# Performance work log

Hardware: AMD Instinct MI355X
Metric: run time of the kernel (lower is better)

The kernel has to match this reference:

```python
import jax, jax.numpy as jnp
import numpy as np

N = 50000
E = 800000
EPS = 1e-16
NEG_SLOPE = 0.2

def setup_inputs() -> dict:
    key = jax.random.key(0)
    ks = jax.random.split(key, 10)
    s = lambda fan: 1.0 / np.sqrt(fan)
    return {
        "x": jax.random.normal(ks[0], (N, 128), dtype=jnp.float32),
        "edge_index": jax.random.randint(ks[1], (2, E), 0, N, dtype=jnp.int64),
        "W1": jax.random.normal(ks[2], (128, 4 * 32), dtype=jnp.float32) * s(128),
        "att_src1": jax.random.normal(ks[3], (4, 32), dtype=jnp.float32) * s(32),
        "att_dst1": jax.random.normal(ks[4], (4, 32), dtype=jnp.float32) * s(32),
        "b1": jnp.zeros((128,), dtype=jnp.float32),
        "W2": jax.random.normal(ks[5], (128, 2), dtype=jnp.float32) * s(128),
        "att_src2": jax.random.normal(ks[6], (1, 2), dtype=jnp.float32) * s(2),
        "att_dst2": jax.random.normal(ks[7], (1, 2), dtype=jnp.float32) * s(2),
        "b2": jnp.zeros((2,), dtype=jnp.float32),
    }

def _gat_conv(x, src, dst, W, att_src, att_dst, bias, heads, out_ch, concat):
    n = x.shape[0]
    h = (x @ W).reshape(n, heads, out_ch)                      # [N,H,C]
    a_src = jnp.sum(h * att_src[None], axis=-1)                # [N,H]
    a_dst = jnp.sum(h * att_dst[None], axis=-1)                # [N,H]
    e = jax.nn.leaky_relu(a_src[src] + a_dst[dst], NEG_SLOPE)  # [Etot,H]
    # segment softmax over incoming edges per destination node
    m = jax.ops.segment_max(e, dst, num_segments=n)            # [N,H]
    m = jnp.where(jnp.isfinite(m), m, 0.0)
    ex = jnp.exp(e - m[dst])
    denom = jax.ops.segment_sum(ex, dst, num_segments=n)       # [N,H]
    alpha = ex / (denom[dst] + EPS)                            # [Etot,H]
    out = jax.ops.segment_sum(alpha[:, :, None] * h[src], dst, num_segments=n)  # [N,H,C]
    if concat:
        out = out.reshape(n, heads * out_ch)
    else:
        out = out.mean(axis=1)
    return out + bias

def reference(x, edge_index, W1, att_src1, att_dst1, b1, W2, att_src2, att_dst2, b2):
    n = x.shape[0]
    # PyG GATConv adds self-loops by default
    loops = jnp.arange(n, dtype=edge_index.dtype)
    src = jnp.concatenate([edge_index[0], loops])
    dst = jnp.concatenate([edge_index[1], loops])
    # dropout is identity at inference
    h = jax.nn.elu(_gat_conv(x, src, dst, W1, att_src1, att_dst1, b1, 4, 32, True))
    h = _gat_conv(h, src, dst, W2, att_src2, att_dst2, b2, 1, 2, False)
    return jax.nn.log_softmax(h, axis=1)
```

## Files before the change

kernel.cpp:

```cpp
#include <hip/hip_runtime.h>
#include <hip/hip_bf16.h>

#define NN 50000
#define EE 800000
#define CAP 64
#define NEG_SLOPE 0.2f
#define EPSF 1e-16f
#define BUILD_BLOCKS 1024
#define GEMM_BLOCKS ((NN + 63) / 64)
#define NPAIRS (EE / 2)
#define WROW 136

typedef unsigned int uint32;
typedef __attribute__((ext_vector_type(8))) short short8;
typedef __attribute__((ext_vector_type(4))) float floatx4;

__device__ __forceinline__ unsigned short f2bf(float f) {
  unsigned int u = __float_as_uint(f);
  unsigned int r = (u + 0x7fffu + ((u >> 16) & 1u)) >> 16;
  return (unsigned short)r;
}
__device__ __forceinline__ float bf_lo(uint32 v) { return __uint_as_float(v << 16); }
__device__ __forceinline__ float bf_hi(uint32 v) { return __uint_as_float(v & 0xffff0000u); }
__device__ __forceinline__ float lrelu(float e) { return fmaxf(e, NEG_SLOPE * e); }

__device__ __forceinline__ void do_build(int b, const int* __restrict__ ei,
                                         int* __restrict__ counts,
                                         int* __restrict__ csr) {
  const int range = b & 7;
  const int lo = range * (NN / 8);
  const int hi = lo + (NN / 8);
  const int group = b >> 3;
  const int tid0 = group * 256 + threadIdx.x;
  const int stride = (BUILD_BLOCKS >> 3) * 256;

  { int n = lo + tid0; if (n < hi) csr[n * CAP] = n; }

  const int2* __restrict__ dst2 = (const int2*)(ei + EE);
  const int2* __restrict__ src2 = (const int2*)(ei);
  for (int p = tid0; p < NPAIRS; p += stride) {
    int2 d2 = dst2[p];
    int2 s2 = src2[p];
    if (d2.x >= lo && d2.x < hi) {
      int r = atomicAdd(&counts[d2.x], 1);
      if (r < CAP - 1) csr[d2.x * CAP + r + 1] = s2.x;
    }
    if (d2.y >= lo && d2.y < hi) {
      int r = atomicAdd(&counts[d2.y], 1);
      if (r < CAP - 1) csr[d2.y * CAP + r + 1] = s2.y;
    }
  }
}

__device__ __forceinline__ void do_gemm_tile(
    int tile, const float* __restrict__ x, const unsigned short* __restrict__ WtL,
    const float* __restrict__ att_src1, const float* __restrict__ att_dst1,
    uint32* __restrict__ h1b, float* __restrict__ as1, float* __restrict__ ad1) {
  const int t    = threadIdx.x;
  const int wave = t >> 6;
  const int lane = t & 63;
  const int quad = lane >> 4;
  const int col  = lane & 15;
  const int nodeBase = tile * 64 + wave * 16;

  floatx4 acc[8];
  #pragma unroll
  for (int i = 0; i < 8; i++) acc[i] = (floatx4){0.f, 0.f, 0.f, 0.f};

  int mread = nodeBase + col; if (mread >= NN) mread = NN - 1;
  const float* __restrict__ xrow = x + (size_t)mread * 128 + quad * 8;
  const unsigned short* __restrict__ bbase = WtL + col * WROW + quad * 8;

  #pragma unroll
  for (int ks = 0; ks < 4; ks++) {
    float4 a0 = *(const float4*)(xrow + ks * 32);
    float4 a1 = *(const float4*)(xrow + ks * 32 + 4);
    union { short8 v; unsigned short u[8]; } af;
    af.u[0] = f2bf(a0.x); af.u[1] = f2bf(a0.y);
    af.u[2] = f2bf(a0.z); af.u[3] = f2bf(a0.w);
    af.u[4] = f2bf(a1.x); af.u[5] = f2bf(a1.y);
    af.u[6] = f2bf(a1.z); af.u[7] = f2bf(a1.w);
    #pragma unroll
    for (int tt = 0; tt < 8; tt++) {
      short8 bf = *(const short8*)(bbase + tt * 16 * WROW + ks * 32);
      acc[tt] = __builtin_amdgcn_mfma_f32_16x16x32_bf16(af.v, bf, acc[tt], 0, 0, 0);
    }
  }

  float asv[8], adv[8];
  #pragma unroll
  for (int tt = 0; tt < 8; tt++) {
    asv[tt] = att_src1[tt * 16 + col];
    adv[tt] = att_dst1[tt * 16 + col];
  }

  #pragma unroll
  for (int r = 0; r < 4; r++) {
    const int gn = nodeBase + quad * 4 + r;
    const bool live = (gn < NN);
    #pragma unroll
    for (int tt = 0; tt < 8; tt++) {
      float v = acc[tt][r];
      float w = __shfl_xor(v, 1, 64);
      if (live && ((col & 1) == 0)) {
        uint32 pk = (uint32)f2bf(v) | ((uint32)f2bf(w) << 16);
        h1b[(size_t)gn * 64 + tt * 8 + (col >> 1)] = pk;
      }
    }
    #pragma unroll
    for (int h = 0; h < 4; h++) {
      float ps = acc[2 * h][r] * asv[2 * h] + acc[2 * h + 1][r] * asv[2 * h + 1];
      float pd = acc[2 * h][r] * adv[2 * h] + acc[2 * h + 1][r] * adv[2 * h + 1];
      #pragma unroll
      for (int off = 1; off < 16; off <<= 1) {
        ps += __shfl_xor(ps, off, 64);
        pd += __shfl_xor(pd, off, 64);
      }
      if (live && col == 0) {
        as1[gn * 4 + h] = ps;
        ad1[gn * 4 + h] = pd;
      }
    }
  }
}

__global__ __launch_bounds__(256) void work_k(
    const int* __restrict__ ei, int* __restrict__ counts, int* __restrict__ csr,
    const float* __restrict__ x, const float* __restrict__ W1,
    const float* __restrict__ att_src1, const float* __restrict__ att_dst1,
    uint32* __restrict__ h1b, float* __restrict__ as1, float* __restrict__ ad1) {
  __shared__ unsigned short WtL[128 * WROW];
  const int b = blockIdx.x;
  if (b < GEMM_BLOCKS) {
    const int c  = threadIdx.x & 127;
    const int kh = (threadIdx.x >> 7) * 4;
    #pragma unroll
    for (int k0 = kh; k0 < 128; k0 += 8) {
      unsigned short w0 = f2bf(W1[(k0 + 0) * 128 + c]);
      unsigned short w1 = f2bf(W1[(k0 + 1) * 128 + c]);
      unsigned short w2 = f2bf(W1[(k0 + 2) * 128 + c]);
      unsigned short w3 = f2bf(W1[(k0 + 3) * 128 + c]);
      uint32 lo = (uint32)w0 | ((uint32)w1 << 16);
      uint32 hi = (uint32)w2 | ((uint32)w3 << 16);
      *(uint2*)&WtL[c * WROW + k0] = make_uint2(lo, hi);
    }
    __syncthreads();
    do_gemm_tile(b, x, WtL, att_src1, att_dst1, h1b, as1, ad1);
  } else {
    do_build(b - GEMM_BLOCKS, ei, counts, csr);
  }
}

__global__ __launch_bounds__(256) void agg1_k(
    const int* __restrict__ counts, const int* __restrict__ csr,
    const uint32* __restrict__ h1b, const float* __restrict__ as1,
    const float* __restrict__ ad1, const float* __restrict__ b1,
    const float* __restrict__ W2, const float* __restrict__ att_src2,
    const float* __restrict__ att_dst2, float4* __restrict__ rec) {
  const int lane = threadIdx.x & 63;
  const int wv = threadIdx.x >> 6;
  const int hd = lane >> 4;
  const int n = __builtin_amdgcn_readfirstlane(blockIdx.x * 4 + wv);

  int cnt = counts[n] + 1;
  cnt = __builtin_amdgcn_readfirstlane(cnt < CAP ? cnt : CAP);
  const int* __restrict__ row = csr + n * CAP;
  const float adv = ad1[n * 4 + hd];

  float den = 0.f, accx = 0.f, accy = 0.f;
  int j = 0;
  for (; j + 3 < cnt; j += 4) {
    int s0 = __builtin_amdgcn_readfirstlane(row[j]);
    int s1 = __builtin_amdgcn_readfirstlane(row[j + 1]);
    int s2 = __builtin_amdgcn_readfirstlane(row[j + 2]);
    int s3 = __builtin_amdgcn_readfirstlane(row[j + 3]);
    float e0 = as1[s0 * 4 + hd] + adv;
    float e1 = as1[s1 * 4 + hd] + adv;
    float e2 = as1[s2 * 4 + hd] + adv;
    float e3 = as1[s3 * 4 + hd] + adv;
    uint32 v0 = h1b[s0 * 64 + lane];
    uint32 v1 = h1b[s1 * 64 + lane];
    uint32 v2 = h1b[s2 * 64 + lane];
    uint32 v3 = h1b[s3 * 64 + lane];
    e0 = lrelu(e0); e1 = lrelu(e1); e2 = lrelu(e2); e3 = lrelu(e3);
    float x0 = __expf(e0), x1 = __expf(e1), x2 = __expf(e2), x3 = __expf(e3);
    den += (x0 + x1) + (x2 + x3);
    accx = fmaf(x0, bf_lo(v0), accx);
    accy = fmaf(x0, bf_hi(v0), accy);
    accx = fmaf(x1, bf_lo(v1), accx);
    accy = fmaf(x1, bf_hi(v1), accy);
    accx = fmaf(x2, bf_lo(v2), accx);
    accy = fmaf(x2, bf_hi(v2), accy);
    accx = fmaf(x3, bf_lo(v3), accx);
    accy = fmaf(x3, bf_hi(v3), accy);
  }
  for (; j < cnt; j++) {
    int s = __builtin_amdgcn_readfirstlane(row[j]);
    float e = lrelu(as1[s * 4 + hd] + adv);
    float ex = __expf(e);
    uint32 v = h1b[s * 64 + lane];
    den += ex;
    accx = fmaf(ex, bf_lo(v), accx);
    accy = fmaf(ex, bf_hi(v), accy);
  }

  float inv = 1.f / (den + EPSF);
  float2 bb = ((const float2*)b1)[lane];
  float ox = accx * inv + bb.x;
  float oy = accy * inv + bb.y;
  ox = (ox > 0.f) ? ox : (__expf(ox) - 1.f);
  oy = (oy > 0.f) ? oy : (__expf(oy) - 1.f);

  float4 wq = ((const float4*)W2)[lane];
  float p0 = ox * wq.x + oy * wq.z;
  float p1 = ox * wq.y + oy * wq.w;
  #pragma unroll
  for (int off = 32; off; off >>= 1) {
    p0 += __shfl_xor(p0, off, 64);
    p1 += __shfl_xor(p1, off, 64);
  }
  if (lane == 0) {
    rec[n] = make_float4(p0, p1,
                         p0 * att_src2[0] + p1 * att_src2[1],
                         p0 * att_dst2[0] + p1 * att_dst2[1]);
  }
}

__global__ __launch_bounds__(256) void agg2_k(
    const int* __restrict__ counts, const int* __restrict__ csr,
    const float4* __restrict__ rec, const float* __restrict__ b2,
    float* __restrict__ out) {
  int i = blockIdx.x * 256 + threadIdx.x;
  if (i >= NN * 8) return;
  int n = i >> 3;
  int sub = i & 7;
  const float adv = rec[n].w;
  int cnt = counts[n] + 1;
  cnt = cnt < CAP ? cnt : CAP;
  const int* __restrict__ row = csr + n * CAP;

  float den = 0.f, a0 = 0.f, a1 = 0.f;
  for (int j = sub; j < cnt; j += 8) {
    int s = row[j];
    float4 rs = rec[s];
    float e = lrelu(rs.z + adv);
    float ex = __expf(e);
    den += ex;
    a0 = fmaf(ex, rs.x, a0);
    a1 = fmaf(ex, rs.y, a1);
  }
  #pragma unroll
  for (int off = 4; off; off >>= 1) {
    den += __shfl_down(den, off, 8);
    a0  += __shfl_down(a0, off, 8);
    a1  += __shfl_down(a1, off, 8);
  }
  if (sub == 0) {
    float inv = 1.f / (den + EPSF);
    float o0 = a0 * inv + b2[0];
    float o1 = a1 * inv + b2[1];
    float mx = fmaxf(o0, o1);
    float lse = mx + __logf(__expf(o0 - mx) + __expf(o1 - mx));
    *(float2*)&out[n * 2] = make_float2(o0 - lse, o1 - lse);
  }
}

extern "C" void kernel_launch(void* const* d_in, const int* in_sizes, int n_in,
                              void* d_out, int out_size, void* d_ws, size_t ws_size,
                              hipStream_t stream) {
  const float* x        = (const float*)d_in[0];
  const int*   ei       = (const int*)d_in[1];
  const float* W1       = (const float*)d_in[2];
  const float* att_src1 = (const float*)d_in[3];
  const float* att_dst1 = (const float*)d_in[4];
  const float* b1       = (const float*)d_in[5];
  const float* W2       = (const float*)d_in[6];
  const float* att_src2 = (const float*)d_in[7];
  const float* att_dst2 = (const float*)d_in[8];
  const float* b2       = (const float*)d_in[9];
  float* out = (float*)d_out;

  char* p = (char*)d_ws;
  auto alloc = [&](size_t bytes) {
    char* r = p;
    p += (bytes + 255) & ~size_t(255);
    return r;
  };
  uint32* h1b  = (uint32*)alloc(sizeof(uint32) * NN * 64);
  float* as1   = (float*)alloc(sizeof(float) * NN * 4);
  float* ad1   = (float*)alloc(sizeof(float) * NN * 4);
  float4* rec  = (float4*)alloc(sizeof(float4) * NN);
  int*   counts = (int*)alloc(sizeof(int) * NN);
  int*   csr   = (int*)alloc(sizeof(int) * NN * CAP);

  hipMemsetAsync(counts, 0, sizeof(int) * NN, stream);
  work_k<<<GEMM_BLOCKS + BUILD_BLOCKS, 256, 0, stream>>>(
      ei, counts, csr, x, W1, att_src1, att_dst1, h1b, as1, ad1);
  agg1_k<<<NN / 4, 256, 0, stream>>>(counts, csr, h1b, as1, ad1, b1, W2,
                                     att_src2, att_dst2, rec);
  agg2_k<<<(NN * 8 + 255) / 256, 256, 0, stream>>>(counts, csr, rec, b2, out);
}
```

Measured before the change: 175.6 us.

## Split wave into four edge groups with 16-byte row loads in layer-1 aggregation

The layer-1 aggregation kernel now has each quarter-wave handle a different incoming edge. Each lane loads a 16-byte chunk (8 bf16 features) of the source row, and partial sums are combined across quarter-waves with shuffles afterwards. This replaces the serial per-edge loop that issued 4-byte loads, aiming for more memory-level parallelism and fewer load instructions per edge. It adds shuffle reductions, masked tail iterations and more registers. Separately, the edge-list reads in the CSR build switch to 64-bit nontemporal loads.

```diff
diff --git a/kernel.cpp b/kernel.cpp
--- a/kernel.cpp
+++ b/kernel.cpp
@@ -36,18 +36,20 @@
 
   { int n = lo + tid0; if (n < hi) csr[n * CAP] = n; }
 
-  const int2* __restrict__ dst2 = (const int2*)(ei + EE);
-  const int2* __restrict__ src2 = (const int2*)(ei);
+  const long long* __restrict__ dst2 = (const long long*)(ei + EE);
+  const long long* __restrict__ src2 = (const long long*)(ei);
   for (int p = tid0; p < NPAIRS; p += stride) {
-    int2 d2 = dst2[p];
-    int2 s2 = src2[p];
-    if (d2.x >= lo && d2.x < hi) {
-      int r = atomicAdd(&counts[d2.x], 1);
-      if (r < CAP - 1) csr[d2.x * CAP + r + 1] = s2.x;
-    }
-    if (d2.y >= lo && d2.y < hi) {
-      int r = atomicAdd(&counts[d2.y], 1);
-      if (r < CAP - 1) csr[d2.y * CAP + r + 1] = s2.y;
+    long long dp = __builtin_nontemporal_load(dst2 + p);
+    long long sp = __builtin_nontemporal_load(src2 + p);
+    int dx = (int)dp, dy = (int)(dp >> 32);
+    int sx = (int)sp, sy = (int)(sp >> 32);
+    if (dx >= lo && dx < hi) {
+      int r = atomicAdd(&counts[dx], 1);
+      if (r < CAP - 1) csr[dx * CAP + r + 1] = sx;
+    }
+    if (dy >= lo && dy < hi) {
+      int r = atomicAdd(&counts[dy], 1);
+      if (r < CAP - 1) csr[dy * CAP + r + 1] = sy;
     }
   }
 }
@@ -158,64 +160,82 @@
     const float* __restrict__ W2, const float* __restrict__ att_src2,
     const float* __restrict__ att_dst2, float4* __restrict__ rec) {
   const int lane = threadIdx.x & 63;
-  const int wv = threadIdx.x >> 6;
-  const int hd = lane >> 4;
+  const int wv   = threadIdx.x >> 6;
+  const int q    = lane >> 4;
+  const int k    = lane & 15;
+  const int hd   = k >> 2;
   const int n = __builtin_amdgcn_readfirstlane(blockIdx.x * 4 + wv);
 
   int cnt = counts[n] + 1;
   cnt = __builtin_amdgcn_readfirstlane(cnt < CAP ? cnt : CAP);
   const int* __restrict__ row = csr + n * CAP;
   const float adv = ad1[n * 4 + hd];
-
-  float den = 0.f, accx = 0.f, accy = 0.f;
-  int j = 0;
-  for (; j + 3 < cnt; j += 4) {
-    int s0 = __builtin_amdgcn_readfirstlane(row[j]);
-    int s1 = __builtin_amdgcn_readfirstlane(row[j + 1]);
-    int s2 = __builtin_amdgcn_readfirstlane(row[j + 2]);
-    int s3 = __builtin_amdgcn_readfirstlane(row[j + 3]);
-    float e0 = as1[s0 * 4 + hd] + adv;
-    float e1 = as1[s1 * 4 + hd] + adv;
-    float e2 = as1[s2 * 4 + hd] + adv;
-    float e3 = as1[s3 * 4 + hd] + adv;
-    uint32 v0 = h1b[s0 * 64 + lane];
-    uint32 v1 = h1b[s1 * 64 + lane];
-    uint32 v2 = h1b[s2 * 64 + lane];
-    uint32 v3 = h1b[s3 * 64 + lane];
-    e0 = lrelu(e0); e1 = lrelu(e1); e2 = lrelu(e2); e3 = lrelu(e3);
-    float x0 = __expf(e0), x1 = __expf(e1), x2 = __expf(e2), x3 = __expf(e3);
-    den += (x0 + x1) + (x2 + x3);
-    accx = fmaf(x0, bf_lo(v0), accx);
-    accy = fmaf(x0, bf_hi(v0), accy);
-    accx = fmaf(x1, bf_lo(v1), accx);
-    accy = fmaf(x1, bf_hi(v1), accy);
-    accx = fmaf(x2, bf_lo(v2), accx);
-    accy = fmaf(x2, bf_hi(v2), accy);
-    accx = fmaf(x3, bf_lo(v3), accx);
-    accy = fmaf(x3, bf_hi(v3), accy);
-  }
-  for (; j < cnt; j++) {
-    int s = __builtin_amdgcn_readfirstlane(row[j]);
+  const uint4* __restrict__ h1v = (const uint4*)h1b;
+
+  float den = 0.f;
+  float a0 = 0.f, a1 = 0.f, a2 = 0.f, a3 = 0.f;
+  float a4 = 0.f, a5 = 0.f, a6 = 0.f, a7 = 0.f;
+
+  for (int base = 0; base < cnt; base += 4) {
+    int j = base + q;
+    bool live = (j < cnt);
+    int s = row[live ? j : base];
     float e = lrelu(as1[s * 4 + hd] + adv);
-    float ex = __expf(e);
-    uint32 v = h1b[s * 64 + lane];
+    float ex = live ? __expf(e) : 0.f;
     den += ex;
-    accx = fmaf(ex, bf_lo(v), accx);
-    accy = fmaf(ex, bf_hi(v), accy);
-  }
+    uint4 v = h1v[(size_t)s * 16 + k];
+    a0 = fmaf(ex, bf_lo(v.x), a0);
+    a1 = fmaf(ex, bf_hi(v.x), a1);
+    a2 = fmaf(ex, bf_lo(v.y), a2);
+    a3 = fmaf(ex, bf_hi(v.y), a3);
+    a4 = fmaf(ex, bf_lo(v.z), a4);
+    a5 = fmaf(ex, bf_hi(v.z), a5);
+    a6 = fmaf(ex, bf_lo(v.w), a6);
+    a7 = fmaf(ex, bf_hi(v.w), a7);
+  }
+
+  den += __shfl_xor(den, 16, 64);
+  den += __shfl_xor(den, 32, 64);
+  a0 += __shfl_xor(a0, 16, 64); a0 += __shfl_xor(a0, 32, 64);
+  a1 += __shfl_xor(a1, 16, 64); a1 += __shfl_xor(a1, 32, 64);
+  a2 += __shfl_xor(a2, 16, 64); a2 += __shfl_xor(a2, 32, 64);
+  a3 += __shfl_xor(a3, 16, 64); a3 += __shfl_xor(a3, 32, 64);
+  a4 += __shfl_xor(a4, 16, 64); a4 += __shfl_xor(a4, 32, 64);
+  a5 += __shfl_xor(a5, 16, 64); a5 += __shfl_xor(a5, 32, 64);
+  a6 += __shfl_xor(a6, 16, 64); a6 += __shfl_xor(a6, 32, 64);
+  a7 += __shfl_xor(a7, 16, 64); a7 += __shfl_xor(a7, 32, 64);
 
   float inv = 1.f / (den + EPSF);
-  float2 bb = ((const float2*)b1)[lane];
-  float ox = accx * inv + bb.x;
-  float oy = accy * inv + bb.y;
-  ox = (ox > 0.f) ? ox : (__expf(ox) - 1.f);
-  oy = (oy > 0.f) ? oy : (__expf(oy) - 1.f);
-
-  float4 wq = ((const float4*)W2)[lane];
-  float p0 = ox * wq.x + oy * wq.z;
-  float p1 = ox * wq.y + oy * wq.w;
-  #pragma unroll
-  for (int off = 32; off; off >>= 1) {
+  float4 bb0 = ((const float4*)b1)[2 * k];
+  float4 bb1 = ((const float4*)b1)[2 * k + 1];
+  float o0 = fmaf(a0, inv, bb0.x);
+  float o1 = fmaf(a1, inv, bb0.y);
+  float o2 = fmaf(a2, inv, bb0.z);
+  float o3 = fmaf(a3, inv, bb0.w);
+  float o4 = fmaf(a4, inv, bb1.x);
+  float o5 = fmaf(a5, inv, bb1.y);
+  float o6 = fmaf(a6, inv, bb1.z);
+  float o7 = fmaf(a7, inv, bb1.w);
+  o0 = (o0 > 0.f) ? o0 : (__expf(o0) - 1.f);
+  o1 = (o1 > 0.f) ? o1 : (__expf(o1) - 1.f);
+  o2 = (o2 > 0.f) ? o2 : (__expf(o2) - 1.f);
+  o3 = (o3 > 0.f) ? o3 : (__expf(o3) - 1.f);
+  o4 = (o4 > 0.f) ? o4 : (__expf(o4) - 1.f);
+  o5 = (o5 > 0.f) ? o5 : (__expf(o5) - 1.f);
+  o6 = (o6 > 0.f) ? o6 : (__expf(o6) - 1.f);
+  o7 = (o7 > 0.f) ? o7 : (__expf(o7) - 1.f);
+
+  const float4* __restrict__ W2v = (const float4*)W2;
+  float4 w0 = W2v[4 * k];
+  float4 w1 = W2v[4 * k + 1];
+  float4 w2 = W2v[4 * k + 2];
+  float4 w3 = W2v[4 * k + 3];
+  float p0 = o0 * w0.x + o1 * w0.z + o2 * w1.x + o3 * w1.z +
+             o4 * w2.x + o5 * w2.z + o6 * w3.x + o7 * w3.z;
+  float p1 = o0 * w0.y + o1 * w0.w + o2 * w1.y + o3 * w1.w +
+             o4 * w2.y + o5 * w2.w + o6 * w3.y + o7 * w3.w;
+  #pragma unroll
+  for (int off = 1; off < 16; off <<= 1) {
     p0 += __shfl_xor(p0, off, 64);
     p1 += __shfl_xor(p1, off, 64);
   }
```

Result: slower. 189.0 us (+7.6%).
